# Kernel optimization log

Measured on AMD Instinct MI355X. Metric: run time of the kernel, lower is better.

Reference implementation:

```python
import jax, jax.numpy as jnp
from jax import lax
import numpy as np

# --- config (torchvision Mask R-CNN RPN / RoIAlign defaults) ---
IMG = 800.0        # image size (square)
STRIDE = 4.0       # FPN level stride -> feature 200x200
K_PRE = 2000       # pre-NMS top-k proposals
K_POST = 512       # post-NMS proposals kept
IOU_THR = 0.7      # RPN NMS IoU threshold
OUT = 7            # RoIAlign output size
SR = 2             # RoIAlign sampling ratio
SCALE = 1.0 / STRIDE
BBOX_XFORM_CLIP = 4.135166556742356  # log(1000/16)


def setup_inputs() -> dict:
    key = jax.random.key(0)
    k1, k2, k3 = jax.random.split(key, 3)
    C, H, W = 256, 200, 200
    feature = jax.random.normal(k1, (C, H, W), jnp.float32)
    # anchor grid: 3 sizes per location, stride 4 (proper geometric anchors)
    sizes = np.array([32.0, 64.0, 128.0], np.float32)
    ys, xs = np.meshgrid(np.arange(H, dtype=np.float32) * STRIDE,
                         np.arange(W, dtype=np.float32) * STRIDE, indexing='ij')
    ctr = np.stack([xs, ys], axis=-1).reshape(-1, 1, 2)            # [HW,1,2] (x,y)
    half = np.stack([sizes / 2, sizes / 2], axis=-1)[None]          # [1,3,2]
    anchors = np.concatenate([ctr - half + 0 * half, ctr + half], axis=-1)
    anchors = np.broadcast_to(np.concatenate([ctr - half, ctr + half], -1),
                              (H * W, 3, 4)).reshape(-1, 4).astype(np.float32)
    N = anchors.shape[0]  # 120000
    objectness = jax.random.normal(k2, (N,), jnp.float32)
    deltas = jax.random.normal(k3, (N, 4), jnp.float32) * 0.1
    return {"feature": feature, "objectness": objectness,
            "deltas": deltas, "anchors": jnp.asarray(anchors)}


def decode_boxes(deltas, anchors):
    w = anchors[:, 2] - anchors[:, 0]
    h = anchors[:, 3] - anchors[:, 1]
    cx = anchors[:, 0] + 0.5 * w
    cy = anchors[:, 1] + 0.5 * h
    dx, dy = deltas[:, 0], deltas[:, 1]
    dw = jnp.minimum(deltas[:, 2], BBOX_XFORM_CLIP)
    dh = jnp.minimum(deltas[:, 3], BBOX_XFORM_CLIP)
    pcx = dx * w + cx
    pcy = dy * h + cy
    pw = jnp.exp(dw) * w
    ph = jnp.exp(dh) * h
    boxes = jnp.stack([pcx - 0.5 * pw, pcy - 0.5 * ph,
                       pcx + 0.5 * pw, pcy + 0.5 * ph], axis=-1)
    return jnp.clip(boxes, 0.0, IMG)


def pairwise_iou(b):  # b: [K,4]
    area = (b[:, 2] - b[:, 0]) * (b[:, 3] - b[:, 1])
    lt = jnp.maximum(b[:, None, :2], b[None, :, :2])
    rb = jnp.minimum(b[:, None, 2:], b[None, :, 2:])
    wh = jnp.maximum(rb - lt, 0.0)
    inter = wh[..., 0] * wh[..., 1]
    return inter / (area[:, None] + area[None, :] - inter + 1e-6)


def nms_suppress(boxes_sorted, iou_thr):
    # boxes sorted by descending score; returns keep mask [K]
    K = boxes_sorted.shape[0]
    iou = pairwise_iou(boxes_sorted)
    js = jnp.arange(K)
    def body(i, supp):
        row = (iou[i] > iou_thr) & (js > i)
        return jnp.where(supp[i], supp, supp | row)
    supp = lax.fori_loop(0, K, body, jnp.zeros((K,), bool))
    return ~supp


def roi_align(feature, boxes):
    # feature: [C,H,W]; boxes: [M,4] in image coords; aligned=False variant
    C, H, W = feature.shape
    P = OUT * SR
    def one(box):
        x1, y1, x2, y2 = box[0] * SCALE, box[1] * SCALE, box[2] * SCALE, box[3] * SCALE
        rw = jnp.maximum(x2 - x1, 1.0)
        rh = jnp.maximum(y2 - y1, 1.0)
        idx = jnp.arange(P, dtype=feature.dtype) + 0.5
        ys = y1 + idx * (rh / P)   # [P]
        xs = x1 + idx * (rw / P)
        yy, xx = jnp.meshgrid(ys, xs, indexing='ij')     # [P,P]
        y = jnp.clip(yy, 0.0, H - 1.0)
        x = jnp.clip(xx, 0.0, W - 1.0)
        y0 = jnp.floor(y).astype(jnp.int32)
        x0 = jnp.floor(x).astype(jnp.int32)
        y1i = jnp.minimum(y0 + 1, H - 1)
        x1i = jnp.minimum(x0 + 1, W - 1)
        ly = y - y0.astype(feature.dtype)
        lx = x - x0.astype(feature.dtype)
        v00 = feature[:, y0, x0]    # [C,P,P]
        v01 = feature[:, y0, x1i]
        v10 = feature[:, y1i, x0]
        v11 = feature[:, y1i, x1i]
        val = (v00 * (1 - ly) * (1 - lx) + v01 * (1 - ly) * lx
               + v10 * ly * (1 - lx) + v11 * ly * lx)  # [C,P,P]
        return val.reshape(C, OUT, SR, OUT, SR).mean(axis=(2, 4))  # [C,7,7]
    return jax.vmap(one)(boxes)


def reference(feature, objectness, deltas, anchors):
    boxes = decode_boxes(deltas, anchors)                    # [N,4]
    scores, idx = lax.top_k(objectness, K_PRE)               # pre-NMS top-k
    cand = boxes[idx]                                        # [K_PRE,4] sorted
    keep = nms_suppress(cand, IOU_THR)                       # [K_PRE] bool
    masked = jnp.where(keep, scores, -jnp.inf)
    _, fidx = lax.top_k(masked, K_POST)                      # post-NMS top-k
    final_boxes = cand[fidx]                                 # [K_POST,4]
    valid = keep[fidx].astype(feature.dtype)                 # [K_POST]
    roi = roi_align(feature, final_boxes)                    # [K_POST,256,7,7]
    return roi * valid[:, None, None, None]
```

## Files before the change

kernel.cpp:

```cpp
#include <hip/hip_runtime.h>
#include <cstdint>
#include <cstddef>

#define N_ANCH   120000
#define K_PRE    2000
#define K_POST   512
#define CAP      4096
#define NWORD    32
#define HBINS    4096
#define IOU_THR  0.7f
#define IMGF     800.0f
#define CLIPV    4.135166556742356f
#define FH       200
#define FW       200
#define FC       256
#define SCALE    0.25f

#define TROWS    96
#define NTILE    21
#define CH       8

#define CG       16
#define TPE      4

typedef unsigned long long u64;
typedef float f2u __attribute__((ext_vector_type(2), aligned(4)));

struct Ws {
    uint32_t T;
    uint32_t cnt;
    int32_t  nk;
    uint32_t pad;
    u64      combo[CAP];
    float4   cand[K_PRE];
    int      rows[K_POST];
    u64      mask[(size_t)K_PRE * NWORD];
};

__device__ inline uint32_t fkey(float f) {
    uint32_t u = __float_as_uint(f);
    return (u & 0x80000000u) ? ~u : (u | 0x80000000u);
}

__global__ __launch_bounds__(1024) void zero_k(Ws* __restrict__ ws) {
    uint32_t* h = (uint32_t*)ws->mask;
    for (int i = threadIdx.x; i < HBINS; i += 1024) h[i] = 0u;
    if (threadIdx.x == 0) { ws->cnt = 0u; ws->nk = 0; ws->T = 0u; }
}

__global__ __launch_bounds__(256) void hist_k(const float* __restrict__ obj,
                                              uint32_t* __restrict__ hist) {
    __shared__ uint32_t h[HBINS];
    for (int i = threadIdx.x; i < HBINS; i += 256) h[i] = 0u;
    __syncthreads();
    const float4* o4 = (const float4*)obj;
    for (int i = blockIdx.x * 256 + threadIdx.x; i < N_ANCH / 4; i += gridDim.x * 256) {
        float4 v = o4[i];
        atomicAdd(&h[fkey(v.x) >> 20], 1u);
        atomicAdd(&h[fkey(v.y) >> 20], 1u);
        atomicAdd(&h[fkey(v.z) >> 20], 1u);
        atomicAdd(&h[fkey(v.w) >> 20], 1u);
    }
    __syncthreads();
    for (int i = threadIdx.x; i < HBINS; i += 256)
        if (h[i]) atomicAdd(&hist[i], h[i]);
}

__global__ __launch_bounds__(256) void gather_k(const float* __restrict__ obj,
                                                const uint32_t* __restrict__ hist,
                                                Ws* __restrict__ ws) {
    __shared__ uint32_t wsum[4];
    __shared__ uint32_t sT;
    const int tid = threadIdx.x;
    const int lane = tid & 63, wave = tid >> 6;
    uint32_t c[16]; uint32_t s = 0;
#pragma unroll
    for (int k = 0; k < 16; ++k) { c[k] = hist[HBINS - 1 - (16 * tid + k)]; s += c[k]; }
    uint32_t incl = s;
    for (int off = 1; off < 64; off <<= 1) {
        uint32_t t = __shfl_up(incl, off);
        if (lane >= off) incl += t;
    }
    if (lane == 63) wsum[wave] = incl;
    __syncthreads();
    uint32_t wpre = 0;
    for (int w2 = 0; w2 < wave; ++w2) wpre += wsum[w2];
    uint32_t before = wpre + incl - s;
#pragma unroll
    for (int k = 0; k < 16; ++k) {
        uint32_t after = before + c[k];
        if (before < K_PRE && after >= K_PRE)
            sT = (uint32_t)(HBINS - 1 - (16 * tid + k)) << 20;
        before = after;
    }
    __syncthreads();
    const uint32_t T = sT;
    int i = blockIdx.x * 256 + tid;
    if (i >= N_ANCH / 4) return;
    float4 v = ((const float4*)obj)[i];
    float vals[4] = {v.x, v.y, v.z, v.w};
#pragma unroll
    for (int k = 0; k < 4; ++k) {
        uint32_t u = fkey(vals[k]);
        if (u >= T) {
            uint32_t pos = atomicAdd(&ws->cnt, 1u);
            if (pos < CAP)
                ws->combo[pos] = ((u64)(~u) << 32) | (uint32_t)(4 * i + k);
        }
    }
}

__global__ __launch_bounds__(256) void rank_decode_k(const float* __restrict__ deltas,
                                                     const float* __restrict__ anchors,
                                                     Ws* __restrict__ ws) {
    __shared__ u64 sc[CAP];
    const int tid = threadIdx.x;
    int M = (int)ws->cnt;
    if (M > CAP) M = CAP;
    const int ebase = blockIdx.x * (256 / TPE);
    if (ebase >= M) return;
    for (int e = tid; e < M; e += 256) sc[e] = ws->combo[e];
    __syncthreads();
    const int gid = ebase + tid / TPE;
    const int sub = tid & (TPE - 1);
    if (gid >= M) return;
    const u64 mine = sc[gid];
    int cnt = 0;
    int j = sub;
    for (; j + 3 * TPE < M; j += 4 * TPE) {
        u64 a = sc[j], b = sc[j + TPE], c = sc[j + 2 * TPE], d = sc[j + 3 * TPE];
        cnt += (int)(a < mine) + (int)(b < mine) + (int)(c < mine) + (int)(d < mine);
    }
    for (; j < M; j += TPE) cnt += (int)(sc[j] < mine);
    cnt += __shfl_xor(cnt, 1);
    cnt += __shfl_xor(cnt, 2);
    if (sub == 0 && cnt < K_PRE) {
        const uint32_t idx = (uint32_t)(mine & 0xFFFFFFFFull);
        float a0 = anchors[idx * 4 + 0], a1 = anchors[idx * 4 + 1];
        float a2 = anchors[idx * 4 + 2], a3 = anchors[idx * 4 + 3];
        float d0 = deltas[idx * 4 + 0],  d1 = deltas[idx * 4 + 1];
        float d2 = fminf(deltas[idx * 4 + 2], CLIPV);
        float d3 = fminf(deltas[idx * 4 + 3], CLIPV);
        float w = a2 - a0, h = a3 - a1;
        float cx = a0 + 0.5f * w, cy = a1 + 0.5f * h;
        float pcx = d0 * w + cx, pcy = d1 * h + cy;
        float pw = expf(d2) * w, ph = expf(d3) * h;
        float x1 = fminf(fmaxf(pcx - 0.5f * pw, 0.0f), IMGF);
        float y1 = fminf(fmaxf(pcy - 0.5f * ph, 0.0f), IMGF);
        float x2 = fminf(fmaxf(pcx + 0.5f * pw, 0.0f), IMGF);
        float y2 = fminf(fmaxf(pcy + 0.5f * ph, 0.0f), IMGF);
        ws->cand[cnt] = make_float4(x1, y1, x2, y2);
    }
}

__global__ __launch_bounds__(256) void nms_mask_k(Ws* __restrict__ ws) {
    const int i = blockIdx.x;
    const int lane = threadIdx.x & 63;
    const int wave = threadIdx.x >> 6;
    const float4 bi = ws->cand[i];
    const float ai = (bi.z - bi.x) * (bi.w - bi.y);
    for (int wd = wave; wd < NWORD; wd += 4) {
        int j = wd * 64 + lane;
        bool bit = false;
        if (j < K_PRE && j > i) {
            float4 bj = ws->cand[j];
            float aj = (bj.z - bj.x) * (bj.w - bj.y);
            float xx1 = fmaxf(bi.x, bj.x);
            float yy1 = fmaxf(bi.y, bj.y);
            float xx2 = fminf(bi.z, bj.z);
            float yy2 = fminf(bi.w, bj.w);
            float ww = fmaxf(xx2 - xx1, 0.0f);
            float hh = fmaxf(yy2 - yy1, 0.0f);
            float inter = ww * hh;
            float iou = inter / (ai + aj - inter + 1e-6f);
            bit = iou > IOU_THR;
        }
        u64 bal = __ballot(bit);
        if (lane == 0) ws->mask[(size_t)i * NWORD + wd] = bal;
    }
}

__global__ __launch_bounds__(512) void nms_scan_k(Ws* __restrict__ ws) {
    __shared__ __align__(16) u64 sbuf[2][TROWS * NWORD];
    __shared__ int s_stop;
    const int tid = threadIdx.x;
    const int lane = tid & 63;
    const int wave = tid >> 6;
    const int lmod = lane & 31;
    const u64* __restrict__ mask = ws->mask;

    {
        const ulonglong2* src = (const ulonglong2*)mask;
        ulonglong2* dst = (ulonglong2*)sbuf[0];
        for (int e = tid; e < TROWS * NWORD / 2; e += 512) dst[e] = src[e];
    }
    if (tid == 0) s_stop = 0;
    __syncthreads();

    u64 supp = 0ull;
    int kcnt = 0;
    int decided = 0;
    for (int t = 0; t < NTILE; ++t) {
        const int base = t * TROWS;
        const int nb = min(TROWS, K_PRE - base);
        if (wave == 0) {
            const u64* sm = sbuf[t & 1];
            u64 A[CH], B[CH];
#pragma unroll
            for (int b = 0; b < CH; ++b) A[b] = sm[b * NWORD + lmod];
            for (int s = 0; s < nb; s += 2 * CH) {
                const bool hasB = (s + CH) < nb;
                if (hasB) {
#pragma unroll
                    for (int b = 0; b < CH; ++b) B[b] = sm[(s + CH + b) * NWORD + lmod];
                }
                {
                    const int w = (base + s) >> 6;
                    const int bofs = (base + s) & 63;
                    u64 keptw = 0ull;
                    if (lane == w) {
                        u64 cur = supp;
#pragma unroll
                        for (int b = 0; b < CH; ++b) {
                            u64 bit = (cur >> (bofs + b)) & 1ull;
                            u64 sel = bit - 1ull;
                            cur |= A[b] & sel;
                            keptw |= sel & (1ull << b);
                        }
                        supp = cur;
                    }
                    u64 kb = __shfl(keptw, w);
                    kcnt += __popcll(kb);
#pragma unroll
                    for (int b = 0; b < CH; ++b) {
                        u64 sel = 0ull - ((kb >> b) & 1ull);
                        supp |= A[b] & sel;
                    }
                }
                if (hasB) {
                    if (s + 2 * CH < nb) {
#pragma unroll
                        for (int b = 0; b < CH; ++b)
                            A[b] = sm[(s + 2 * CH + b) * NWORD + lmod];
                    }
                    const int w = (base + s + CH) >> 6;
                    const int bofs = (base + s + CH) & 63;
                    u64 keptw = 0ull;
                    if (lane == w) {
                        u64 cur = supp;
#pragma unroll
                        for (int b = 0; b < CH; ++b) {
                            u64 bit = (cur >> (bofs + b)) & 1ull;
                            u64 sel = bit - 1ull;
                            cur |= B[b] & sel;
                            keptw |= sel & (1ull << b);
                        }
                        supp = cur;
                    }
                    u64 kb = __shfl(keptw, w);
                    kcnt += __popcll(kb);
#pragma unroll
                    for (int b = 0; b < CH; ++b) {
                        u64 sel = 0ull - ((kb >> b) & 1ull);
                        supp |= B[b] & sel;
                    }
                }
            }
            decided = base + nb;
            if (lane == 0 && kcnt >= K_POST) s_stop = 1;
        } else if (t + 1 < NTILE) {
            const int nbase = (t + 1) * TROWS;
            const int npairs = (min(TROWS, K_PRE - nbase) * NWORD) / 2;
            const ulonglong2* src = (const ulonglong2*)(mask + (size_t)nbase * NWORD);
            ulonglong2* dst = (ulonglong2*)sbuf[(t + 1) & 1];
            for (int e = tid - 64; e < npairs; e += 448) dst[e] = src[e];
        }
        __syncthreads();
        if (s_stop) break;
    }

    if (wave == 0) {
        u64 valid;
        if (lane < NWORD - 1)       valid = ~0ull;
        else if (lane == NWORD - 1) valid = (1ull << (K_PRE - (NWORD - 1) * 64)) - 1ull;
        else                        valid = 0ull;
        const int dw = decided - lane * 64;
        const u64 dmask = (dw <= 0) ? 0ull : ((dw >= 64) ? ~0ull : ((1ull << dw) - 1ull));
        u64 keepw = (~supp) & valid & dmask;
        int cnt = __popcll(keepw);
        int incl = cnt;
        for (int off = 1; off < 64; off <<= 1) {
            int t = __shfl_up(incl, off);
            if (lane >= off) incl += t;
        }
        int pos = incl - cnt;
        u64 kw = keepw;
        while (kw) {
            int b = __ffsll((unsigned long long)kw) - 1;
            kw &= kw - 1ull;
            if (pos < K_POST) ws->rows[pos] = lane * 64 + b;
            ++pos;
        }
        int total = __shfl(incl, 63);
        if (lane == 0) ws->nk = total;
        int start = total < K_POST ? total : K_POST;
        for (int r = start + lane; r < K_POST; r += 64) ws->rows[r] = -1;
    }
}

__global__ __launch_bounds__(256) void roi_k(const float* __restrict__ feat,
                                             const Ws* __restrict__ ws,
                                             float* __restrict__ out) {
    const int b = blockIdx.x;
    const int xcd = b & 7;
    const int s = b >> 3;
    const int r = s & (K_POST - 1);
    const int cg = xcd + 8 * (s >> 9);
    const int cbase = cg * CG;
    float* oblk = out + (size_t)r * (FC * 49) + (size_t)cbase * 49;
    const int row = ws->rows[r];
    const int tid = threadIdx.x;

    if (row < 0) {
        for (int e = tid; e < CG * 49; e += 256) oblk[e] = 0.0f;
        return;
    }
    if (tid >= 245) return;

    const int p = tid % 49;
    const int cslot = tid / 49;
    const int oy = p / 7, ox = p % 7;

    const float4 bx = ws->cand[row];
    const float x1 = bx.x * SCALE, y1 = bx.y * SCALE;
    const float x2 = bx.z * SCALE, y2 = bx.w * SCALE;
    const float rw = fmaxf(x2 - x1, 1.0f);
    const float rh = fmaxf(y2 - y1, 1.0f);
    const float stepx = rw / 14.0f;
    const float stepy = rh / 14.0f;

    int    off0[4], off1[4];
    float4 w4[4];
#pragma unroll
    for (int sub = 0; sub < 4; ++sub) {
        const int sy = sub >> 1, sx = sub & 1;
        float yy = y1 + ((float)(2 * oy + sy) + 0.5f) * stepy;
        float y = fminf(fmaxf(yy, 0.0f), (float)(FH - 1));
        float fy0 = floorf(y);
        int iy0 = (int)fy0;
        int iy1 = min(iy0 + 1, FH - 1);
        float ly = y - fy0;
        float xx = x1 + ((float)(2 * ox + sx) + 0.5f) * stepx;
        float x = fminf(fmaxf(xx, 0.0f), (float)(FW - 1));
        float fx0 = floorf(x);
        int ix0 = (int)fx0;
        float lx = x - fx0;
        float wxl, wxr; int base;
        if (ix0 >= FW - 1) { base = FW - 2; wxl = 0.0f; wxr = 1.0f; }
        else               { base = ix0;    wxl = 1.0f - lx; wxr = lx; }
        float wy0 = 1.0f - ly, wy1 = ly;
        off0[sub] = iy0 * FW + base;
        off1[sub] = iy1 * FW + base;
        w4[sub] = make_float4(wy0 * wxl * 0.25f, wy0 * wxr * 0.25f,
                              wy1 * wxl * 0.25f, wy1 * wxr * 0.25f);
    }

    const float* fb = feat + (size_t)cbase * (FH * FW);
    const float* f0 = fb + (size_t)cslot * (FH * FW);
    const float* f1 = fb + (size_t)(cslot + 5) * (FH * FW);
    const float* f2 = fb + (size_t)(cslot + 10) * (FH * FW);
    f2u r0[8], r1[8], r2[8], r3[8];
#pragma unroll
    for (int sub = 0; sub < 4; ++sub) {
        r0[2 * sub]     = *(const f2u*)(f0 + off0[sub]);
        r0[2 * sub + 1] = *(const f2u*)(f0 + off1[sub]);
    }
#pragma unroll
    for (int sub = 0; sub < 4; ++sub) {
        r1[2 * sub]     = *(const f2u*)(f1 + off0[sub]);
        r1[2 * sub + 1] = *(const f2u*)(f1 + off1[sub]);
    }
#pragma unroll
    for (int sub = 0; sub < 4; ++sub) {
        r2[2 * sub]     = *(const f2u*)(f2 + off0[sub]);
        r2[2 * sub + 1] = *(const f2u*)(f2 + off1[sub]);
    }
    const bool has4 = (cslot == 0);
    if (has4) {
        const float* f3 = fb + (size_t)15 * (FH * FW);
#pragma unroll
        for (int sub = 0; sub < 4; ++sub) {
            r3[2 * sub]     = *(const f2u*)(f3 + off0[sub]);
            r3[2 * sub + 1] = *(const f2u*)(f3 + off1[sub]);
        }
    }

    float a0 = 0.0f, a1 = 0.0f, a2 = 0.0f;
#pragma unroll
    for (int sub = 0; sub < 4; ++sub) {
        a0 += w4[sub].x * r0[2 * sub].x + w4[sub].y * r0[2 * sub].y
            + w4[sub].z * r0[2 * sub + 1].x + w4[sub].w * r0[2 * sub + 1].y;
    }
#pragma unroll
    for (int sub = 0; sub < 4; ++sub) {
        a1 += w4[sub].x * r1[2 * sub].x + w4[sub].y * r1[2 * sub].y
            + w4[sub].z * r1[2 * sub + 1].x + w4[sub].w * r1[2 * sub + 1].y;
    }
#pragma unroll
    for (int sub = 0; sub < 4; ++sub) {
        a2 += w4[sub].x * r2[2 * sub].x + w4[sub].y * r2[2 * sub].y
            + w4[sub].z * r2[2 * sub + 1].x + w4[sub].w * r2[2 * sub + 1].y;
    }
    oblk[cslot * 49 + p] = a0;
    oblk[(cslot + 5) * 49 + p] = a1;
    oblk[(cslot + 10) * 49 + p] = a2;

    if (has4) {
        float a3 = 0.0f;
#pragma unroll
        for (int sub = 0; sub < 4; ++sub) {
            a3 += w4[sub].x * r3[2 * sub].x + w4[sub].y * r3[2 * sub].y
                + w4[sub].z * r3[2 * sub + 1].x + w4[sub].w * r3[2 * sub + 1].y;
        }
        oblk[15 * 49 + p] = a3;
    }
}

extern "C" void kernel_launch(void* const* d_in, const int* in_sizes, int n_in,
                              void* d_out, int out_size, void* d_ws, size_t ws_size,
                              hipStream_t stream) {
    const float* feature    = (const float*)d_in[0];
    const float* objectness = (const float*)d_in[1];
    const float* deltas     = (const float*)d_in[2];
    const float* anchors    = (const float*)d_in[3];
    Ws* ws = (Ws*)d_ws;
    uint32_t* hist = (uint32_t*)ws->mask;
    float* out = (float*)d_out;

    hipLaunchKernelGGL(zero_k, dim3(1), dim3(1024), 0, stream, ws);
    hipLaunchKernelGGL(hist_k, dim3(256), dim3(256), 0, stream, objectness, hist);
    hipLaunchKernelGGL(gather_k, dim3((N_ANCH / 4 + 255) / 256), dim3(256), 0, stream,
                       objectness, hist, ws);
    hipLaunchKernelGGL(rank_decode_k, dim3(CAP / (256 / TPE)), dim3(256), 0, stream,
                       deltas, anchors, ws);
    hipLaunchKernelGGL(nms_mask_k, dim3(K_PRE), dim3(256), 0, stream, ws);
    hipLaunchKernelGGL(nms_scan_k, dim3(1), dim3(512), 0, stream, ws);
    hipLaunchKernelGGL(roi_k, dim3(16 * K_POST), dim3(256), 0, stream, feature, ws, out);
}
```

Before: 195.2 us.

## Fuse all RPN and RoIAlign stages into one cooperative persistent kernel

```diff
diff --git a/kernel.cpp b/kernel.cpp
--- a/kernel.cpp
+++ b/kernel.cpp
@@ -1,6 +1,9 @@
 #include <hip/hip_runtime.h>
+#include <hip/hip_cooperative_groups.h>
 #include <cstdint>
 #include <cstddef>
+
+namespace cgrp = cooperative_groups;
 
 #define N_ANCH   120000
 #define K_PRE    2000
@@ -42,387 +45,392 @@
     return (u & 0x80000000u) ? ~u : (u | 0x80000000u);
 }
 
-__global__ __launch_bounds__(1024) void zero_k(Ws* __restrict__ ws) {
-    uint32_t* h = (uint32_t*)ws->mask;
-    for (int i = threadIdx.x; i < HBINS; i += 1024) h[i] = 0u;
-    if (threadIdx.x == 0) { ws->cnt = 0u; ws->nk = 0; ws->T = 0u; }
-}
-
-__global__ __launch_bounds__(256) void hist_k(const float* __restrict__ obj,
-                                              uint32_t* __restrict__ hist) {
-    __shared__ uint32_t h[HBINS];
-    for (int i = threadIdx.x; i < HBINS; i += 256) h[i] = 0u;
-    __syncthreads();
-    const float4* o4 = (const float4*)obj;
-    for (int i = blockIdx.x * 256 + threadIdx.x; i < N_ANCH / 4; i += gridDim.x * 256) {
-        float4 v = o4[i];
-        atomicAdd(&h[fkey(v.x) >> 20], 1u);
-        atomicAdd(&h[fkey(v.y) >> 20], 1u);
-        atomicAdd(&h[fkey(v.z) >> 20], 1u);
-        atomicAdd(&h[fkey(v.w) >> 20], 1u);
-    }
-    __syncthreads();
-    for (int i = threadIdx.x; i < HBINS; i += 256)
-        if (h[i]) atomicAdd(&hist[i], h[i]);
-}
-
-__global__ __launch_bounds__(256) void gather_k(const float* __restrict__ obj,
-                                                const uint32_t* __restrict__ hist,
-                                                Ws* __restrict__ ws) {
-    __shared__ uint32_t wsum[4];
-    __shared__ uint32_t sT;
-    const int tid = threadIdx.x;
-    const int lane = tid & 63, wave = tid >> 6;
-    uint32_t c[16]; uint32_t s = 0;
-#pragma unroll
-    for (int k = 0; k < 16; ++k) { c[k] = hist[HBINS - 1 - (16 * tid + k)]; s += c[k]; }
-    uint32_t incl = s;
-    for (int off = 1; off < 64; off <<= 1) {
-        uint32_t t = __shfl_up(incl, off);
-        if (lane >= off) incl += t;
-    }
-    if (lane == 63) wsum[wave] = incl;
-    __syncthreads();
-    uint32_t wpre = 0;
-    for (int w2 = 0; w2 < wave; ++w2) wpre += wsum[w2];
-    uint32_t before = wpre + incl - s;
-#pragma unroll
-    for (int k = 0; k < 16; ++k) {
-        uint32_t after = before + c[k];
-        if (before < K_PRE && after >= K_PRE)
-            sT = (uint32_t)(HBINS - 1 - (16 * tid + k)) << 20;
-        before = after;
-    }
-    __syncthreads();
-    const uint32_t T = sT;
-    int i = blockIdx.x * 256 + tid;
-    if (i >= N_ANCH / 4) return;
-    float4 v = ((const float4*)obj)[i];
-    float vals[4] = {v.x, v.y, v.z, v.w};
-#pragma unroll
-    for (int k = 0; k < 4; ++k) {
-        uint32_t u = fkey(vals[k]);
-        if (u >= T) {
-            uint32_t pos = atomicAdd(&ws->cnt, 1u);
-            if (pos < CAP)
-                ws->combo[pos] = ((u64)(~u) << 32) | (uint32_t)(4 * i + k);
-        }
-    }
-}
-
-__global__ __launch_bounds__(256) void rank_decode_k(const float* __restrict__ deltas,
-                                                     const float* __restrict__ anchors,
-                                                     Ws* __restrict__ ws) {
-    __shared__ u64 sc[CAP];
-    const int tid = threadIdx.x;
-    int M = (int)ws->cnt;
-    if (M > CAP) M = CAP;
-    const int ebase = blockIdx.x * (256 / TPE);
-    if (ebase >= M) return;
-    for (int e = tid; e < M; e += 256) sc[e] = ws->combo[e];
-    __syncthreads();
-    const int gid = ebase + tid / TPE;
-    const int sub = tid & (TPE - 1);
-    if (gid >= M) return;
-    const u64 mine = sc[gid];
-    int cnt = 0;
-    int j = sub;
-    for (; j + 3 * TPE < M; j += 4 * TPE) {
-        u64 a = sc[j], b = sc[j + TPE], c = sc[j + 2 * TPE], d = sc[j + 3 * TPE];
-        cnt += (int)(a < mine) + (int)(b < mine) + (int)(c < mine) + (int)(d < mine);
-    }
-    for (; j < M; j += TPE) cnt += (int)(sc[j] < mine);
-    cnt += __shfl_xor(cnt, 1);
-    cnt += __shfl_xor(cnt, 2);
-    if (sub == 0 && cnt < K_PRE) {
-        const uint32_t idx = (uint32_t)(mine & 0xFFFFFFFFull);
-        float a0 = anchors[idx * 4 + 0], a1 = anchors[idx * 4 + 1];
-        float a2 = anchors[idx * 4 + 2], a3 = anchors[idx * 4 + 3];
-        float d0 = deltas[idx * 4 + 0],  d1 = deltas[idx * 4 + 1];
-        float d2 = fminf(deltas[idx * 4 + 2], CLIPV);
-        float d3 = fminf(deltas[idx * 4 + 3], CLIPV);
-        float w = a2 - a0, h = a3 - a1;
-        float cx = a0 + 0.5f * w, cy = a1 + 0.5f * h;
-        float pcx = d0 * w + cx, pcy = d1 * h + cy;
-        float pw = expf(d2) * w, ph = expf(d3) * h;
-        float x1 = fminf(fmaxf(pcx - 0.5f * pw, 0.0f), IMGF);
-        float y1 = fminf(fmaxf(pcy - 0.5f * ph, 0.0f), IMGF);
-        float x2 = fminf(fmaxf(pcx + 0.5f * pw, 0.0f), IMGF);
-        float y2 = fminf(fmaxf(pcy + 0.5f * ph, 0.0f), IMGF);
-        ws->cand[cnt] = make_float4(x1, y1, x2, y2);
-    }
-}
-
-__global__ __launch_bounds__(256) void nms_mask_k(Ws* __restrict__ ws) {
-    const int i = blockIdx.x;
-    const int lane = threadIdx.x & 63;
-    const int wave = threadIdx.x >> 6;
-    const float4 bi = ws->cand[i];
-    const float ai = (bi.z - bi.x) * (bi.w - bi.y);
-    for (int wd = wave; wd < NWORD; wd += 4) {
-        int j = wd * 64 + lane;
-        bool bit = false;
-        if (j < K_PRE && j > i) {
-            float4 bj = ws->cand[j];
-            float aj = (bj.z - bj.x) * (bj.w - bj.y);
-            float xx1 = fmaxf(bi.x, bj.x);
-            float yy1 = fmaxf(bi.y, bj.y);
-            float xx2 = fminf(bi.z, bj.z);
-            float yy2 = fminf(bi.w, bj.w);
-            float ww = fmaxf(xx2 - xx1, 0.0f);
-            float hh = fmaxf(yy2 - yy1, 0.0f);
-            float inter = ww * hh;
-            float iou = inter / (ai + aj - inter + 1e-6f);
-            bit = iou > IOU_THR;
-        }
-        u64 bal = __ballot(bit);
-        if (lane == 0) ws->mask[(size_t)i * NWORD + wd] = bal;
-    }
-}
-
-__global__ __launch_bounds__(512) void nms_scan_k(Ws* __restrict__ ws) {
-    __shared__ __align__(16) u64 sbuf[2][TROWS * NWORD];
-    __shared__ int s_stop;
-    const int tid = threadIdx.x;
+union __align__(16) Smem {
+    uint32_t hist[HBINS];
+    struct { uint32_t wsum[4]; uint32_t sT; } res;
+    u64 sc[CAP];
+    struct { u64 buf[2][TROWS * NWORD]; int stop; } scan;
+};
+
+__global__ __launch_bounds__(256, 3) void fused_k(const float* __restrict__ feat,
+                                                  const float* __restrict__ obj,
+                                                  const float* __restrict__ deltas,
+                                                  const float* __restrict__ anchors,
+                                                  Ws* __restrict__ ws,
+                                                  float* __restrict__ out) {
+    cgrp::grid_group grid = cgrp::this_grid();
+    __shared__ Smem sm;
+    const int tid  = threadIdx.x;
+    const int bid  = blockIdx.x;
+    const int NB   = gridDim.x;
     const int lane = tid & 63;
     const int wave = tid >> 6;
-    const int lmod = lane & 31;
-    const u64* __restrict__ mask = ws->mask;
+    uint32_t* hist = (uint32_t*)ws->mask;
+
+    for (int i = bid * 256 + tid; i < HBINS; i += NB * 256) hist[i] = 0u;
+    if (bid == 0 && tid == 0) { ws->cnt = 0u; ws->nk = 0; }
+    grid.sync();
 
     {
-        const ulonglong2* src = (const ulonglong2*)mask;
-        ulonglong2* dst = (ulonglong2*)sbuf[0];
-        for (int e = tid; e < TROWS * NWORD / 2; e += 512) dst[e] = src[e];
-    }
-    if (tid == 0) s_stop = 0;
-    __syncthreads();
-
-    u64 supp = 0ull;
-    int kcnt = 0;
-    int decided = 0;
-    for (int t = 0; t < NTILE; ++t) {
-        const int base = t * TROWS;
-        const int nb = min(TROWS, K_PRE - base);
-        if (wave == 0) {
-            const u64* sm = sbuf[t & 1];
-            u64 A[CH], B[CH];
-#pragma unroll
-            for (int b = 0; b < CH; ++b) A[b] = sm[b * NWORD + lmod];
-            for (int s = 0; s < nb; s += 2 * CH) {
-                const bool hasB = (s + CH) < nb;
-                if (hasB) {
-#pragma unroll
-                    for (int b = 0; b < CH; ++b) B[b] = sm[(s + CH + b) * NWORD + lmod];
+        for (int i = tid; i < HBINS; i += 256) sm.hist[i] = 0u;
+        __syncthreads();
+        const float4* o4 = (const float4*)obj;
+        for (int i = bid * 256 + tid; i < N_ANCH / 4; i += NB * 256) {
+            float4 v = o4[i];
+            atomicAdd(&sm.hist[fkey(v.x) >> 20], 1u);
+            atomicAdd(&sm.hist[fkey(v.y) >> 20], 1u);
+            atomicAdd(&sm.hist[fkey(v.z) >> 20], 1u);
+            atomicAdd(&sm.hist[fkey(v.w) >> 20], 1u);
+        }
+        __syncthreads();
+        for (int i = tid; i < HBINS; i += 256)
+            if (sm.hist[i]) atomicAdd(&hist[i], sm.hist[i]);
+    }
+    grid.sync();
+
+    if (bid * 256 < N_ANCH / 4) {
+        uint32_t c[16]; uint32_t s = 0;
+#pragma unroll
+        for (int k = 0; k < 16; ++k) { c[k] = hist[HBINS - 1 - (16 * tid + k)]; s += c[k]; }
+        uint32_t incl = s;
+        for (int off = 1; off < 64; off <<= 1) {
+            uint32_t t = __shfl_up(incl, off);
+            if (lane >= off) incl += t;
+        }
+        if (lane == 63) sm.res.wsum[wave] = incl;
+        __syncthreads();
+        uint32_t wpre = 0;
+        for (int w2 = 0; w2 < wave; ++w2) wpre += sm.res.wsum[w2];
+        uint32_t before = wpre + incl - s;
+#pragma unroll
+        for (int k = 0; k < 16; ++k) {
+            uint32_t after = before + c[k];
+            if (before < K_PRE && after >= K_PRE)
+                sm.res.sT = (uint32_t)(HBINS - 1 - (16 * tid + k)) << 20;
+            before = after;
+        }
+        __syncthreads();
+        const uint32_t T = sm.res.sT;
+        const int i = bid * 256 + tid;
+        if (i < N_ANCH / 4) {
+            float4 v = ((const float4*)obj)[i];
+            float vals[4] = {v.x, v.y, v.z, v.w};
+#pragma unroll
+            for (int k = 0; k < 4; ++k) {
+                uint32_t u = fkey(vals[k]);
+                if (u >= T) {
+                    uint32_t pos = atomicAdd(&ws->cnt, 1u);
+                    if (pos < CAP)
+                        ws->combo[pos] = ((u64)(~u) << 32) | (uint32_t)(4 * i + k);
                 }
-                {
-                    const int w = (base + s) >> 6;
-                    const int bofs = (base + s) & 63;
-                    u64 keptw = 0ull;
-                    if (lane == w) {
-                        u64 cur = supp;
+            }
+        }
+    }
+    grid.sync();
+
+    if (bid < CAP / (256 / TPE)) {
+        int M = (int)ws->cnt;
+        if (M > CAP) M = CAP;
+        const int ebase = bid * (256 / TPE);
+        if (ebase < M) {
+            for (int e = tid; e < M; e += 256) sm.sc[e] = ws->combo[e];
+            __syncthreads();
+            const int gid = ebase + tid / TPE;
+            const int sub = tid & (TPE - 1);
+            if (gid < M) {
+                const u64 mine = sm.sc[gid];
+                int cnt = 0;
+                int j = sub;
+                for (; j + 3 * TPE < M; j += 4 * TPE) {
+                    u64 a = sm.sc[j], b = sm.sc[j + TPE];
+                    u64 c2 = sm.sc[j + 2 * TPE], d = sm.sc[j + 3 * TPE];
+                    cnt += (int)(a < mine) + (int)(b < mine) + (int)(c2 < mine) + (int)(d < mine);
+                }
+                for (; j < M; j += TPE) cnt += (int)(sm.sc[j] < mine);
+                cnt += __shfl_xor(cnt, 1);
+                cnt += __shfl_xor(cnt, 2);
+                if (sub == 0 && cnt < K_PRE) {
+                    const uint32_t idx = (uint32_t)(mine & 0xFFFFFFFFull);
+                    float a0 = anchors[idx * 4 + 0], a1 = anchors[idx * 4 + 1];
+                    float a2 = anchors[idx * 4 + 2], a3 = anchors[idx * 4 + 3];
+                    float d0 = deltas[idx * 4 + 0],  d1 = deltas[idx * 4 + 1];
+                    float d2 = fminf(deltas[idx * 4 + 2], CLIPV);
+                    float d3 = fminf(deltas[idx * 4 + 3], CLIPV);
+                    float w = a2 - a0, h = a3 - a1;
+                    float cx = a0 + 0.5f * w, cy = a1 + 0.5f * h;
+                    float pcx = d0 * w + cx, pcy = d1 * h + cy;
+                    float pw = expf(d2) * w, ph = expf(d3) * h;
+                    float x1 = fminf(fmaxf(pcx - 0.5f * pw, 0.0f), IMGF);
+                    float y1 = fminf(fmaxf(pcy - 0.5f * ph, 0.0f), IMGF);
+                    float x2 = fminf(fmaxf(pcx + 0.5f * pw, 0.0f), IMGF);
+                    float y2 = fminf(fmaxf(pcy + 0.5f * ph, 0.0f), IMGF);
+                    ws->cand[cnt] = make_float4(x1, y1, x2, y2);
+                }
+            }
+        }
+    }
+    grid.sync();
+
+    for (int i = bid; i < K_PRE; i += NB) {
+        const float4 bi = ws->cand[i];
+        const float ai = (bi.z - bi.x) * (bi.w - bi.y);
+        for (int wd = wave; wd < NWORD; wd += 4) {
+            int j = wd * 64 + lane;
+            bool bit = false;
+            if (j < K_PRE && j > i) {
+                float4 bj = ws->cand[j];
+                float aj = (bj.z - bj.x) * (bj.w - bj.y);
+                float xx1 = fmaxf(bi.x, bj.x);
+                float yy1 = fmaxf(bi.y, bj.y);
+                float xx2 = fminf(bi.z, bj.z);
+                float yy2 = fminf(bi.w, bj.w);
+                float ww = fmaxf(xx2 - xx1, 0.0f);
+                float hh = fmaxf(yy2 - yy1, 0.0f);
+                float inter = ww * hh;
+                float iou = inter / (ai + aj - inter + 1e-6f);
+                bit = iou > IOU_THR;
+            }
+            u64 bal = __ballot(bit);
+            if (lane == 0) ws->mask[(size_t)i * NWORD + wd] = bal;
+        }
+    }
+    grid.sync();
+
+    if (bid == 0) {
+        const int lmod = lane & 31;
+        const u64* __restrict__ mask = ws->mask;
+        {
+            const ulonglong2* src = (const ulonglong2*)mask;
+            ulonglong2* dst = (ulonglong2*)sm.scan.buf[0];
+            for (int e = tid; e < TROWS * NWORD / 2; e += 256) dst[e] = src[e];
+        }
+        if (tid == 0) sm.scan.stop = 0;
+        __syncthreads();
+
+        u64 supp = 0ull;
+        int kcnt = 0;
+        int decided = 0;
+        for (int t = 0; t < NTILE; ++t) {
+            const int base = t * TROWS;
+            const int nb = min(TROWS, K_PRE - base);
+            if (wave == 0) {
+                const u64* smb = sm.scan.buf[t & 1];
+                u64 A[CH], B[CH];
+#pragma unroll
+                for (int b = 0; b < CH; ++b) A[b] = smb[b * NWORD + lmod];
+                for (int s = 0; s < nb; s += 2 * CH) {
+                    const bool hasB = (s + CH) < nb;
+                    if (hasB) {
+#pragma unroll
+                        for (int b = 0; b < CH; ++b) B[b] = smb[(s + CH + b) * NWORD + lmod];
+                    }
+                    {
+                        const int w = (base + s) >> 6;
+                        const int bofs = (base + s) & 63;
+                        u64 keptw = 0ull;
+                        if (lane == w) {
+                            u64 cur = supp;
+#pragma unroll
+                            for (int b = 0; b < CH; ++b) {
+                                u64 bit = (cur >> (bofs + b)) & 1ull;
+                                u64 sel = bit - 1ull;
+                                cur |= A[b] & sel;
+                                keptw |= sel & (1ull << b);
+                            }
+                            supp = cur;
+                        }
+                        u64 kb = __shfl(keptw, w);
+                        kcnt += __popcll(kb);
 #pragma unroll
                         for (int b = 0; b < CH; ++b) {
-                            u64 bit = (cur >> (bofs + b)) & 1ull;
-                            u64 sel = bit - 1ull;
-                            cur |= A[b] & sel;
-                            keptw |= sel & (1ull << b);
+                            u64 sel = 0ull - ((kb >> b) & 1ull);
+                            supp |= A[b] & sel;
                         }
-                        supp = cur;
                     }
-                    u64 kb = __shfl(keptw, w);
-                    kcnt += __popcll(kb);
-#pragma unroll
-                    for (int b = 0; b < CH; ++b) {
-                        u64 sel = 0ull - ((kb >> b) & 1ull);
-                        supp |= A[b] & sel;
+                    if (hasB) {
+                        if (s + 2 * CH < nb) {
+#pragma unroll
+                            for (int b = 0; b < CH; ++b)
+                                A[b] = smb[(s + 2 * CH + b) * NWORD + lmod];
+                        }
+                        const int w = (base + s + CH) >> 6;
+                        const int bofs = (base + s + CH) & 63;
+                        u64 keptw = 0ull;
+                        if (lane == w) {
+                            u64 cur = supp;
+#pragma unroll
+                            for (int b = 0; b < CH; ++b) {
+                                u64 bit = (cur >> (bofs + b)) & 1ull;
+                                u64 sel = bit - 1ull;
+                                cur |= B[b] & sel;
+                                keptw |= sel & (1ull << b);
+                            }
+                            supp = cur;
+                        }
+                        u64 kb = __shfl(keptw, w);
+                        kcnt += __popcll(kb);
+#pragma unroll
+                        for (int b = 0; b < CH; ++b) {
+                            u64 sel = 0ull - ((kb >> b) & 1ull);
+                            supp |= B[b] & sel;
+                        }
                     }
                 }
-                if (hasB) {
-                    if (s + 2 * CH < nb) {
-#pragma unroll
-                        for (int b = 0; b < CH; ++b)
-                            A[b] = sm[(s + 2 * CH + b) * NWORD + lmod];
-                    }
-                    const int w = (base + s + CH) >> 6;
-                    const int bofs = (base + s + CH) & 63;
-                    u64 keptw = 0ull;
-                    if (lane == w) {
-                        u64 cur = supp;
-#pragma unroll
-                        for (int b = 0; b < CH; ++b) {
-                            u64 bit = (cur >> (bofs + b)) & 1ull;
-                            u64 sel = bit - 1ull;
-                            cur |= B[b] & sel;
-                            keptw |= sel & (1ull << b);
-                        }
-                        supp = cur;
-                    }
-                    u64 kb = __shfl(keptw, w);
-                    kcnt += __popcll(kb);
-#pragma unroll
-                    for (int b = 0; b < CH; ++b) {
-                        u64 sel = 0ull - ((kb >> b) & 1ull);
-                        supp |= B[b] & sel;
-                    }
-                }
-            }
-            decided = base + nb;
-            if (lane == 0 && kcnt >= K_POST) s_stop = 1;
-        } else if (t + 1 < NTILE) {
-            const int nbase = (t + 1) * TROWS;
-            const int npairs = (min(TROWS, K_PRE - nbase) * NWORD) / 2;
-            const ulonglong2* src = (const ulonglong2*)(mask + (size_t)nbase * NWORD);
-            ulonglong2* dst = (ulonglong2*)sbuf[(t + 1) & 1];
-            for (int e = tid - 64; e < npairs; e += 448) dst[e] = src[e];
-        }
-        __syncthreads();
-        if (s_stop) break;
-    }
-
-    if (wave == 0) {
-        u64 valid;
-        if (lane < NWORD - 1)       valid = ~0ull;
-        else if (lane == NWORD - 1) valid = (1ull << (K_PRE - (NWORD - 1) * 64)) - 1ull;
-        else                        valid = 0ull;
-        const int dw = decided - lane * 64;
-        const u64 dmask = (dw <= 0) ? 0ull : ((dw >= 64) ? ~0ull : ((1ull << dw) - 1ull));
-        u64 keepw = (~supp) & valid & dmask;
-        int cnt = __popcll(keepw);
-        int incl = cnt;
-        for (int off = 1; off < 64; off <<= 1) {
-            int t = __shfl_up(incl, off);
-            if (lane >= off) incl += t;
-        }
-        int pos = incl - cnt;
-        u64 kw = keepw;
-        while (kw) {
-            int b = __ffsll((unsigned long long)kw) - 1;
-            kw &= kw - 1ull;
-            if (pos < K_POST) ws->rows[pos] = lane * 64 + b;
-            ++pos;
-        }
-        int total = __shfl(incl, 63);
-        if (lane == 0) ws->nk = total;
-        int start = total < K_POST ? total : K_POST;
-        for (int r = start + lane; r < K_POST; r += 64) ws->rows[r] = -1;
-    }
-}
-
-__global__ __launch_bounds__(256) void roi_k(const float* __restrict__ feat,
-                                             const Ws* __restrict__ ws,
-                                             float* __restrict__ out) {
-    const int b = blockIdx.x;
-    const int xcd = b & 7;
-    const int s = b >> 3;
-    const int r = s & (K_POST - 1);
-    const int cg = xcd + 8 * (s >> 9);
-    const int cbase = cg * CG;
-    float* oblk = out + (size_t)r * (FC * 49) + (size_t)cbase * 49;
-    const int row = ws->rows[r];
-    const int tid = threadIdx.x;
-
-    if (row < 0) {
-        for (int e = tid; e < CG * 49; e += 256) oblk[e] = 0.0f;
-        return;
-    }
-    if (tid >= 245) return;
-
-    const int p = tid % 49;
-    const int cslot = tid / 49;
-    const int oy = p / 7, ox = p % 7;
-
-    const float4 bx = ws->cand[row];
-    const float x1 = bx.x * SCALE, y1 = bx.y * SCALE;
-    const float x2 = bx.z * SCALE, y2 = bx.w * SCALE;
-    const float rw = fmaxf(x2 - x1, 1.0f);
-    const float rh = fmaxf(y2 - y1, 1.0f);
-    const float stepx = rw / 14.0f;
-    const float stepy = rh / 14.0f;
-
-    int    off0[4], off1[4];
-    float4 w4[4];
-#pragma unroll
-    for (int sub = 0; sub < 4; ++sub) {
-        const int sy = sub >> 1, sx = sub & 1;
-        float yy = y1 + ((float)(2 * oy + sy) + 0.5f) * stepy;
-        float y = fminf(fmaxf(yy, 0.0f), (float)(FH - 1));
-        float fy0 = floorf(y);
-        int iy0 = (int)fy0;
-        int iy1 = min(iy0 + 1, FH - 1);
-        float ly = y - fy0;
-        float xx = x1 + ((float)(2 * ox + sx) + 0.5f) * stepx;
-        float x = fminf(fmaxf(xx, 0.0f), (float)(FW - 1));
-        float fx0 = floorf(x);
-        int ix0 = (int)fx0;
-        float lx = x - fx0;
-        float wxl, wxr; int base;
-        if (ix0 >= FW - 1) { base = FW - 2; wxl = 0.0f; wxr = 1.0f; }
-        else               { base = ix0;    wxl = 1.0f - lx; wxr = lx; }
-        float wy0 = 1.0f - ly, wy1 = ly;
-        off0[sub] = iy0 * FW + base;
-        off1[sub] = iy1 * FW + base;
-        w4[sub] = make_float4(wy0 * wxl * 0.25f, wy0 * wxr * 0.25f,
-                              wy1 * wxl * 0.25f, wy1 * wxr * 0.25f);
-    }
-
-    const float* fb = feat + (size_t)cbase * (FH * FW);
-    const float* f0 = fb + (size_t)cslot * (FH * FW);
-    const float* f1 = fb + (size_t)(cslot + 5) * (FH * FW);
-    const float* f2 = fb + (size_t)(cslot + 10) * (FH * FW);
-    f2u r0[8], r1[8], r2[8], r3[8];
-#pragma unroll
-    for (int sub = 0; sub < 4; ++sub) {
-        r0[2 * sub]     = *(const f2u*)(f0 + off0[sub]);
-        r0[2 * sub + 1] = *(const f2u*)(f0 + off1[sub]);
-    }
-#pragma unroll
-    for (int sub = 0; sub < 4; ++sub) {
-        r1[2 * sub]     = *(const f2u*)(f1 + off0[sub]);
-        r1[2 * sub + 1] = *(const f2u*)(f1 + off1[sub]);
-    }
-#pragma unroll
-    for (int sub = 0; sub < 4; ++sub) {
-        r2[2 * sub]     = *(const f2u*)(f2 + off0[sub]);
-        r2[2 * sub + 1] = *(const f2u*)(f2 + off1[sub]);
-    }
-    const bool has4 = (cslot == 0);
-    if (has4) {
-        const float* f3 = fb + (size_t)15 * (FH * FW);
-#pragma unroll
-        for (int sub = 0; sub < 4; ++sub) {
-            r3[2 * sub]     = *(const f2u*)(f3 + off0[sub]);
-            r3[2 * sub + 1] = *(const f2u*)(f3 + off1[sub]);
-        }
-    }
-
-    float a0 = 0.0f, a1 = 0.0f, a2 = 0.0f;
-#pragma unroll
-    for (int sub = 0; sub < 4; ++sub) {
-        a0 += w4[sub].x * r0[2 * sub].x + w4[sub].y * r0[2 * sub].y
-            + w4[sub].z * r0[2 * sub + 1].x + w4[sub].w * r0[2 * sub + 1].y;
-    }
-#pragma unroll
-    for (int sub = 0; sub < 4; ++sub) {
-        a1 += w4[sub].x * r1[2 * sub].x + w4[sub].y * r1[2 * sub].y
-            + w4[sub].z * r1[2 * sub + 1].x + w4[sub].w * r1[2 * sub + 1].y;
-    }
-#pragma unroll
-    for (int sub = 0; sub < 4; ++sub) {
-        a2 += w4[sub].x * r2[2 * sub].x + w4[sub].y * r2[2 * sub].y
-            + w4[sub].z * r2[2 * sub + 1].x + w4[sub].w * r2[2 * sub + 1].y;
-    }
-    oblk[cslot * 49 + p] = a0;
-    oblk[(cslot + 5) * 49 + p] = a1;
-    oblk[(cslot + 10) * 49 + p] = a2;
-
-    if (has4) {
-        float a3 = 0.0f;
-#pragma unroll
-        for (int sub = 0; sub < 4; ++sub) {
-            a3 += w4[sub].x * r3[2 * sub].x + w4[sub].y * r3[2 * sub].y
-                + w4[sub].z * r3[2 * sub + 1].x + w4[sub].w * r3[2 * sub + 1].y;
-        }
-        oblk[15 * 49 + p] = a3;
+                decided = base + nb;
+                if (lane == 0 && kcnt >= K_POST) sm.scan.stop = 1;
+            } else if (t + 1 < NTILE) {
+                const int nbase = (t + 1) * TROWS;
+                const int npairs = (min(TROWS, K_PRE - nbase) * NWORD) / 2;
+                const ulonglong2* src = (const ulonglong2*)(mask + (size_t)nbase * NWORD);
+                ulonglong2* dst = (ulonglong2*)sm.scan.buf[(t + 1) & 1];
+                for (int e = tid - 64; e < npairs; e += 192) dst[e] = src[e];
+            }
+            __syncthreads();
+            if (sm.scan.stop) break;
+        }
+
+        if (wave == 0) {
+            u64 valid;
+            if (lane < NWORD - 1)       valid = ~0ull;
+            else if (lane == NWORD - 1) valid = (1ull << (K_PRE - (NWORD - 1) * 64)) - 1ull;
+            else                        valid = 0ull;
+            const int dw = decided - lane * 64;
+            const u64 dmask = (dw <= 0) ? 0ull : ((dw >= 64) ? ~0ull : ((1ull << dw) - 1ull));
+            u64 keepw = (~supp) & valid & dmask;
+            int cnt = __popcll(keepw);
+            int incl = cnt;
+            for (int off = 1; off < 64; off <<= 1) {
+                int t = __shfl_up(incl, off);
+                if (lane >= off) incl += t;
+            }
+            int pos = incl - cnt;
+            u64 kw = keepw;
+            while (kw) {
+                int b = __ffsll((unsigned long long)kw) - 1;
+                kw &= kw - 1ull;
+                if (pos < K_POST) ws->rows[pos] = lane * 64 + b;
+                ++pos;
+            }
+            int total = __shfl(incl, 63);
+            if (lane == 0) ws->nk = total;
+            int start = total < K_POST ? total : K_POST;
+            for (int r = start + lane; r < K_POST; r += 64) ws->rows[r] = -1;
+        }
+    }
+    grid.sync();
+
+    for (int vb = bid; vb < 16 * K_POST; vb += NB) {
+        const int xcd = vb & 7;
+        const int sq = vb >> 3;
+        const int r = sq & (K_POST - 1);
+        const int cgi = xcd + 8 * (sq >> 9);
+        const int cbase = cgi * CG;
+        float* oblk = out + (size_t)r * (FC * 49) + (size_t)cbase * 49;
+        const int row = ws->rows[r];
+
+        if (row < 0) {
+            for (int e = tid; e < CG * 49; e += 256) oblk[e] = 0.0f;
+            continue;
+        }
+        if (tid >= 245) continue;
+
+        const int p = tid % 49;
+        const int cslot = tid / 49;
+        const int oy = p / 7, ox = p % 7;
+
+        const float4 bx = ws->cand[row];
+        const float x1 = bx.x * SCALE, y1 = bx.y * SCALE;
+        const float x2 = bx.z * SCALE, y2 = bx.w * SCALE;
+        const float rw = fmaxf(x2 - x1, 1.0f);
+        const float rh = fmaxf(y2 - y1, 1.0f);
+        const float stepx = rw / 14.0f;
+        const float stepy = rh / 14.0f;
+
+        int    off0[4], off1[4];
+        float4 w4[4];
+#pragma unroll
+        for (int sub = 0; sub < 4; ++sub) {
+            const int sy = sub >> 1, sx = sub & 1;
+            float yy = y1 + ((float)(2 * oy + sy) + 0.5f) * stepy;
+            float y = fminf(fmaxf(yy, 0.0f), (float)(FH - 1));
+            float fy0 = floorf(y);
+            int iy0 = (int)fy0;
+            int iy1 = min(iy0 + 1, FH - 1);
+            float ly = y - fy0;
+            float xx = x1 + ((float)(2 * ox + sx) + 0.5f) * stepx;
+            float x = fminf(fmaxf(xx, 0.0f), (float)(FW - 1));
+            float fx0 = floorf(x);
+            int ix0 = (int)fx0;
+            float lx = x - fx0;
+            float wxl, wxr; int base;
+            if (ix0 >= FW - 1) { base = FW - 2; wxl = 0.0f; wxr = 1.0f; }
+            else               { base = ix0;    wxl = 1.0f - lx; wxr = lx; }
+            float wy0 = 1.0f - ly, wy1 = ly;
+            off0[sub] = iy0 * FW + base;
+            off1[sub] = iy1 * FW + base;
+            w4[sub] = make_float4(wy0 * wxl * 0.25f, wy0 * wxr * 0.25f,
+                                  wy1 * wxl * 0.25f, wy1 * wxr * 0.25f);
+        }
+
+        const float* fb = feat + (size_t)cbase * (FH * FW);
+        const float* f0 = fb + (size_t)cslot * (FH * FW);
+        const float* f1 = fb + (size_t)(cslot + 5) * (FH * FW);
+        const float* f2 = fb + (size_t)(cslot + 10) * (FH * FW);
+        f2u r0[8], r1[8], r2[8], r3[8];
+#pragma unroll
+        for (int sub = 0; sub < 4; ++sub) {
+            r0[2 * sub]     = *(const f2u*)(f0 + off0[sub]);
+            r0[2 * sub + 1] = *(const f2u*)(f0 + off1[sub]);
+        }
+#pragma unroll
+        for (int sub = 0; sub < 4; ++sub) {
+            r1[2 * sub]     = *(const f2u*)(f1 + off0[sub]);
+            r1[2 * sub + 1] = *(const f2u*)(f1 + off1[sub]);
+        }
+#pragma unroll
+        for (int sub = 0; sub < 4; ++sub) {
+            r2[2 * sub]     = *(const f2u*)(f2 + off0[sub]);
+            r2[2 * sub + 1] = *(const f2u*)(f2 + off1[sub]);
+        }
+        const bool has4 = (cslot == 0);
+        if (has4) {
+            const float* f3 = fb + (size_t)15 * (FH * FW);
+#pragma unroll
+            for (int sub = 0; sub < 4; ++sub) {
+                r3[2 * sub]     = *(const f2u*)(f3 + off0[sub]);
+                r3[2 * sub + 1] = *(const f2u*)(f3 + off1[sub]);
+            }
+        }
+
+        float a0 = 0.0f, a1 = 0.0f, a2 = 0.0f;
+#pragma unroll
+        for (int sub = 0; sub < 4; ++sub) {
+            a0 += w4[sub].x * r0[2 * sub].x + w4[sub].y * r0[2 * sub].y
+                + w4[sub].z * r0[2 * sub + 1].x + w4[sub].w * r0[2 * sub + 1].y;
+        }
+#pragma unroll
+        for (int sub = 0; sub < 4; ++sub) {
+            a1 += w4[sub].x * r1[2 * sub].x + w4[sub].y * r1[2 * sub].y
+                + w4[sub].z * r1[2 * sub + 1].x + w4[sub].w * r1[2 * sub + 1].y;
+        }
+#pragma unroll
+        for (int sub = 0; sub < 4; ++sub) {
+            a2 += w4[sub].x * r2[2 * sub].x + w4[sub].y * r2[2 * sub].y
+                + w4[sub].z * r2[2 * sub + 1].x + w4[sub].w * r2[2 * sub + 1].y;
+        }
+        oblk[cslot * 49 + p] = a0;
+        oblk[(cslot + 5) * 49 + p] = a1;
+        oblk[(cslot + 10) * 49 + p] = a2;
+
+        if (has4) {
+            float a3 = 0.0f;
+#pragma unroll
+            for (int sub = 0; sub < 4; ++sub) {
+                a3 += w4[sub].x * r3[2 * sub].x + w4[sub].y * r3[2 * sub].y
+                    + w4[sub].z * r3[2 * sub + 1].x + w4[sub].w * r3[2 * sub + 1].y;
+            }
+            oblk[15 * 49 + p] = a3;
+        }
     }
 }
 
@@ -434,16 +442,23 @@
     const float* deltas     = (const float*)d_in[2];
     const float* anchors    = (const float*)d_in[3];
     Ws* ws = (Ws*)d_ws;
-    uint32_t* hist = (uint32_t*)ws->mask;
     float* out = (float*)d_out;
 
-    hipLaunchKernelGGL(zero_k, dim3(1), dim3(1024), 0, stream, ws);
-    hipLaunchKernelGGL(hist_k, dim3(256), dim3(256), 0, stream, objectness, hist);
-    hipLaunchKernelGGL(gather_k, dim3((N_ANCH / 4 + 255) / 256), dim3(256), 0, stream,
-                       objectness, hist, ws);
-    hipLaunchKernelGGL(rank_decode_k, dim3(CAP / (256 / TPE)), dim3(256), 0, stream,
-                       deltas, anchors, ws);
-    hipLaunchKernelGGL(nms_mask_k, dim3(K_PRE), dim3(256), 0, stream, ws);
-    hipLaunchKernelGGL(nms_scan_k, dim3(1), dim3(512), 0, stream, ws);
-    hipLaunchKernelGGL(roi_k, dim3(16 * K_POST), dim3(256), 0, stream, feature, ws, out);
+    static int s_grid = 0;
+    if (s_grid == 0) {
+        int nb = 0;
+        if (hipOccupancyMaxActiveBlocksPerMultiprocessor(&nb, fused_k, 256, 0) != hipSuccess || nb < 1)
+            nb = 1;
+        if (nb > 3) nb = 3;
+        int ncu = 256;
+        hipDeviceProp_t prop;
+        if (hipGetDeviceProperties(&prop, 0) == hipSuccess && prop.multiProcessorCount > 0)
+            ncu = prop.multiProcessorCount;
+        s_grid = (nb * ncu) & ~7;
+        if (s_grid < 8) s_grid = 8;
+    }
+
+    void* args[] = {(void*)&feature, (void*)&objectness, (void*)&deltas,
+                    (void*)&anchors, (void*)&ws, (void*)&out};
+    hipLaunchCooperativeKernel(fused_k, dim3(s_grid), dim3(256), args, 0, stream);
 }
```

Result: slower. 500.5 us (+156.4%).
